# Kernel optimization log

Hardware: AMD Instinct MI355X
Metric: run time of the kernel (lower is better)

The kernel has to match this reference:

```python
import jax, jax.numpy as jnp
import numpy as np

T, B, C, U = 4000, 64, 64, 200
NEG_INF = jnp.float32(-1e30)


def setup_inputs() -> dict:
    key = jax.random.key(0)
    k1, k2 = jax.random.split(key)
    inputs = jax.random.normal(k1, (T, B, C), dtype=jnp.float32)  # time-major logits
    targets = jax.random.randint(k2, (B, U), 0, C, dtype=jnp.int32)
    return {"inputs": inputs, "targets": targets}


def reference(inputs, targets):
    # Transducer.forward: transitions is None -> log_softmax over classes.
    log_probs = jax.nn.log_softmax(inputs, axis=-1)  # [T, B, C]
    # emit[t, b, u] = log_probs[t, b, targets[b, u]]
    b_idx = jnp.arange(B)[:, None]  # [B, 1]
    emit = log_probs[:, b_idx, targets]  # [T, B, U]

    # ASG-style monotone alignment forward DP (no blank, repeats collapse):
    # alpha[t, u] = emit[t, u] + logsumexp(alpha[t-1, u], alpha[t-1, u-1])
    alpha0 = jnp.full((B, U), NEG_INF, dtype=inputs.dtype).at[:, 0].set(emit[0, :, 0])

    def step(alpha, emit_t):
        shifted = jnp.concatenate(
            [jnp.full((B, 1), NEG_INF, dtype=alpha.dtype), alpha[:, :-1]], axis=1
        )
        return emit_t + jnp.logaddexp(alpha, shifted), None

    alpha_T, _ = jax.lax.scan(step, alpha0, emit[1:])  # scan over T-1 frames
    losses = -alpha_T[:, U - 1]  # negated forward score per sample
    return jnp.mean(losses)  # TransducerLossFunction returns torch.mean(loss)
```

## Files before the change

### kernel.cpp

```cpp
#include <hip/hip_runtime.h>

#define T_DIM 4000
#define B_DIM 64
#define C_DIM 64
#define U_DIM 200
#define LOG2E 1.4426950408889634f
#define LN2 0.6931471805599453f

#define PAIRS 2000
#define PB_BYTES (PAIRS * 800)
#define NSLOT 20

__device__ __forceinline__ float hw_exp2(float x) { return __builtin_amdgcn_exp2f(x); }
__device__ __forceinline__ float hw_log2(float x) { return __builtin_amdgcn_logf(x); }

template <int CTRL>
__device__ __forceinline__ int dpp_i(int x) {
    return __builtin_amdgcn_update_dpp(0, x, CTRL, 0xF, 0xF, true);
}
template <int CTRL>
__device__ __forceinline__ float dpp_f(float x) {
    return __uint_as_float((unsigned)dpp_i<CTRL>((int)__float_as_uint(x)));
}

__device__ __forceinline__ unsigned rne_bf16(float v) {
    unsigned b = __float_as_uint(v);
    return b + 0x7FFFu + ((b >> 16) & 1u);
}

__global__ __launch_bounds__(256, 8) void prep_kernel(const float* __restrict__ in,
                                                      const int* __restrict__ tgt,
                                                      unsigned* __restrict__ eg,
                                                      float* __restrict__ out) {
    __shared__ unsigned short exh[16 * 8 * 68];
    __shared__ unsigned tgc[400];
    __shared__ float red[4];
    const int tid = threadIdx.x;
    const int bg = blockIdx.x & 7;
    const int tc = blockIdx.x >> 3;
    const int t0 = tc * 16, b0 = bg * 8;

    for (int o = tid; o < 400; o += 256) {
        int4 tv = ((const int4*)tgt)[bg * 400 + o];
        tgc[o] = (unsigned)(tv.x & 63) | ((unsigned)(tv.y & 63) << 8)
               | ((unsigned)(tv.z & 63) << 16) | ((unsigned)(tv.w & 63) << 24);
    }
    #pragma unroll
    for (int k = 0; k < 8; ++k) {
        int flat = k * 256 + tid;
        int t_l = flat >> 7, i = flat & 127, b_l = i >> 4, q = i & 15;
        float4 v = *(const float4*)(in + (size_t)(t0 + t_l) * 4096 + (b0 + b_l) * 64 + q * 4);
        unsigned ex0 = rne_bf16(hw_exp2(v.x * LOG2E));
        unsigned ex1 = rne_bf16(hw_exp2(v.y * LOG2E));
        unsigned ex2 = rne_bf16(hw_exp2(v.z * LOG2E));
        unsigned ex3 = rne_bf16(hw_exp2(v.w * LOG2E));
        uint2 pk;
        pk.x = (ex0 >> 16) | (ex1 & 0xFFFF0000u);
        pk.y = (ex2 >> 16) | (ex3 & 0xFFFF0000u);
        *(uint2*)&exh[(t_l * 8 + b_l) * 68 + q * 4] = pk;
    }
    __syncthreads();

    {
        float v = 0.0f;
        if (tid < 128) {
            const unsigned* p = (const unsigned*)&exh[tid * 68];
            float s = 0.0f;
            #pragma unroll
            for (int j = 0; j < 32; ++j) {
                unsigned u = p[j];
                s += __uint_as_float(u << 16) + __uint_as_float(u & 0xFFFF0000u);
            }
            v = hw_log2(s);
        }
        #pragma unroll
        for (int o = 32; o > 0; o >>= 1) v += __shfl_xor(v, o);
        if ((tid & 63) == 0) red[tid >> 6] = v;
    }

    {
        const int wv4 = tid >> 6;
        const int ln = tid & 63;
        for (int r = wv4; r < 64; r += 4) {
            int b_l = r & 7, tp_l = r >> 3;
            if (ln < 50) {
                unsigned tw = tgc[b_l * 50 + ln];
                int c0 = tw & 255, c1 = (tw >> 8) & 255, c2 = (tw >> 16) & 255, c3 = tw >> 24;
                const unsigned short* plo = &exh[(tp_l * 16 + b_l) * 68];
                const unsigned short* phi = plo + 8 * 68;
                uint4 w;
                w.x = (unsigned)plo[c0] | ((unsigned)plo[c1] << 16);
                w.y = (unsigned)plo[c2] | ((unsigned)plo[c3] << 16);
                w.z = (unsigned)phi[c0] | ((unsigned)phi[c1] << 16);
                w.w = (unsigned)phi[c2] | ((unsigned)phi[c3] << 16);
                *(uint4*)((char*)eg + (size_t)(b0 + b_l) * PB_BYTES
                          + (size_t)(tc * 8 + tp_l) * 800 + ln * 16) = w;
            }
        }
    }
    __syncthreads();
    if (tid == 0)
        atomicAdd(out, (red[0] + red[1] + red[2] + red[3]) * (LN2 / 64.0f));
}

struct ScanState { float A0, A1, A2, A3; int S, D; };

__device__ __forceinline__ void renorm(ScanState& st, int lane) {
    float m = fmaxf(fmaxf(st.A0, st.A1), fmaxf(st.A2, st.A3));
    int e = (int)((__float_as_uint(m) >> 23) & 0xFFu);
    int cand = st.S + e - 127;
    int snb = dpp_i<0x138>(st.S);
    if (lane == 0) snb = -(1 << 28);
    int snew = max(cand, snb);
    int k = st.S - snew;
    st.A0 = ldexpf(st.A0, k);
    st.A1 = ldexpf(st.A1, k);
    st.A2 = ldexpf(st.A2, k);
    st.A3 = ldexpf(st.A3, k);
    st.S = snew;
    st.D = min(dpp_i<0x138>(snew) - snew, 60);
}

__device__ __forceinline__ void step(ScanState& st, float e0, float e1, float e2, float e3) {
    float sh = ldexpf(dpp_f<0x138>(st.A3), st.D);
    sh = fminf(sh, 1.125899906842624e15f);
    float t0 = st.A0 + sh;
    float t1 = st.A1 + st.A0;
    float t2 = st.A2 + st.A1;
    float t3 = st.A3 + st.A2;
    st.A0 = e0 * t0; st.A1 = e1 * t1; st.A2 = e2 * t2; st.A3 = e3 * t3;
}

__device__ __forceinline__ void brenorm(ScanState& st) {
    float m = fmaxf(fmaxf(st.A0, st.A1), fmaxf(st.A2, st.A3));
    int e = (int)((__float_as_uint(m) >> 23) & 0xFFu);
    int cand = st.S + e - 127;
    int snb = dpp_i<0x130>(st.S);
    int snew = max(cand, snb);
    int k = st.S - snew;
    st.A0 = ldexpf(st.A0, k);
    st.A1 = ldexpf(st.A1, k);
    st.A2 = ldexpf(st.A2, k);
    st.A3 = ldexpf(st.A3, k);
    st.S = snew;
    st.D = min(dpp_i<0x130>(snew) - snew, 60);
}

__device__ __forceinline__ void bstep(ScanState& st, float e0, float e1, float e2, float e3) {
    float e4s = fminf(ldexpf(dpp_f<0x130>(e0), st.D), 1.125899906842624e15f);
    float b0n = dpp_f<0x130>(st.A0);
    float g0 = e0 * st.A0, g1 = e1 * st.A1, g2 = e2 * st.A2, g3 = e3 * st.A3;
    st.A0 = g0 + g1; st.A1 = g1 + g2; st.A2 = g2 + g3; st.A3 = g3 + e4s * b0n;
}

__device__ __forceinline__ ScanState scan_init(const float* in, const int* tgt, int lane, int b) {
    float v0 = in[b * 64 + (tgt[b * U_DIM] & 63)];
    ScanState st;
    st.A0 = (lane == 0) ? hw_exp2(v0 * LOG2E) : 0.0f;
    st.A1 = 0.0f; st.A2 = 0.0f; st.A3 = 0.0f;
    st.S = 0; st.D = 0;
    return st;
}

#define LO(x) __uint_as_float((x) << 16)
#define HI(x) __uint_as_float((x) & 0xFFFF0000u)

__global__ __launch_bounds__(128, 1) void scan2_kernel(const float* __restrict__ in,
                                                       const int* __restrict__ tgt,
                                                       const unsigned* __restrict__ eg,
                                                       float* __restrict__ out) {
    __shared__ float jb0[64], jb1[64], jb2[64], jb3[64];
    __shared__ int jsb[64];
    const int lane = threadIdx.x & 63;
    const int wv = threadIdx.x >> 6;
    const int b = blockIdx.x;
    const int lidx = (lane < 50) ? lane : 49;
    const char* egb = (const char*)eg + (size_t)b * PB_BYTES;

    ScanState st;
    if (wv == 1) {
        st.A0 = 0.0f; st.A1 = 0.0f; st.A2 = 0.0f;
        st.A3 = (lane == 49) ? 1.0f : 0.0f;
        st.S = 0; st.D = 0;
        int off = 1999 * 800 + lidx * 16;
        uint4 wb[NSLOT];
        #pragma unroll
        for (int j = 0; j < NSLOT; ++j) { wb[j] = *(const uint4*)(egb + off); off -= 800; }
        for (int k = 0; k < 49; ++k) {
            #pragma unroll
            for (int j = 0; j < NSLOT; ++j) {
                if ((j & 3) == 0) brenorm(st);
                uint4 w = wb[j];
                wb[j] = *(const uint4*)(egb + off); off -= 800;
                bstep(st, LO(w.z), HI(w.z), LO(w.w), HI(w.w));
                bstep(st, LO(w.x), HI(w.x), LO(w.y), HI(w.y));
            }
        }
        #pragma unroll
        for (int j = 0; j < NSLOT; ++j) {
            if ((j & 3) == 0) brenorm(st);
            uint4 w = wb[j];
            bstep(st, LO(w.z), HI(w.z), LO(w.w), HI(w.w));
            if (j < NSLOT - 1) bstep(st, LO(w.x), HI(w.x), LO(w.y), HI(w.y));
        }
        brenorm(st);
        jb0[lane] = st.A0; jb1[lane] = st.A1; jb2[lane] = st.A2; jb3[lane] = st.A3;
        jsb[lane] = st.S;
    } else {
        st = scan_init(in, tgt, lane, b);
        int off = 800 + lidx * 16;
        uint4 wb[NSLOT];
        #pragma unroll
        for (int j = 0; j < NSLOT; ++j) { wb[j] = *(const uint4*)(egb + off); off += 800; }
        uint2 h0 = *(const uint2*)(egb + lidx * 16 + 8);
        step(st, LO(h0.x), HI(h0.x), LO(h0.y), HI(h0.y));
        for (int k = 0; k < 49; ++k) {
            #pragma unroll
            for (int j = 0; j < NSLOT; ++j) {
                if ((j & 3) == 0) renorm(st, lane);
                uint4 w = wb[j];
                wb[j] = *(const uint4*)(egb + off); off += 800;
                step(st, LO(w.x), HI(w.x), LO(w.y), HI(w.y));
                step(st, LO(w.z), HI(w.z), LO(w.w), HI(w.w));
            }
        }
        #pragma unroll
        for (int j = 0; j < NSLOT; ++j) {
            if ((j & 3) == 0) renorm(st, lane);
            uint4 w = wb[j];
            step(st, LO(w.x), HI(w.x), LO(w.y), HI(w.y));
            if (j < NSLOT - 1) step(st, LO(w.z), HI(w.z), LO(w.w), HI(w.w));
        }
        renorm(st, lane);
    }
    __syncthreads();
    if (wv == 0) {
        float d = st.A0 * jb0[lane] + st.A1 * jb1[lane]
                + st.A2 * jb2[lane] + st.A3 * jb3[lane];
        float ll = (lane < 50) ? hw_log2(fmaxf(d, 1e-38f)) + (float)(st.S + jsb[lane])
                               : -1e30f;
        float mx = ll;
        #pragma unroll
        for (int o = 32; o > 0; o >>= 1) mx = fmaxf(mx, __shfl_xor(mx, o));
        float s = (lane < 50) ? hw_exp2(ll - mx) : 0.0f;
        #pragma unroll
        for (int o = 32; o > 0; o >>= 1) s += __shfl_xor(s, o);
        if (lane == 0) atomicAdd(out, -(mx + hw_log2(s)) * (LN2 / 64.0f));
    }
}

__global__ __launch_bounds__(256) void lse_sum_kernel(const float* __restrict__ in,
                                                      float* __restrict__ out) {
    const int lane = threadIdx.x & 63;
    const int w = threadIdx.x >> 6;
    const int wid = blockIdx.x * 4 + w;
    const int ROWS = (T_DIM * B_DIM) / 1024;
    const float* p = in + (size_t)wid * ROWS * 64 + lane;
    float acc = 0.0f;
    for (int i = 0; i < ROWS; i += 2) {
        float xa = p[(size_t)i * 64];
        float xb = p[(size_t)(i + 1) * 64];
        float ea = hw_exp2(xa * LOG2E);
        float eb = hw_exp2(xb * LOG2E);
        #pragma unroll
        for (int off = 32; off > 0; off >>= 1) {
            ea += __shfl_xor(ea, off);
            eb += __shfl_xor(eb, off);
        }
        acc += hw_log2(ea) + hw_log2(eb);
    }
    __shared__ float red[4];
    if (lane == 0) red[w] = acc;
    __syncthreads();
    if (threadIdx.x == 0)
        atomicAdd(out, (red[0] + red[1] + red[2] + red[3]) * (LN2 / 64.0f));
}

__global__ __launch_bounds__(64) void scan_fb(const float* __restrict__ in,
                                              const int* __restrict__ tgt,
                                              float* __restrict__ out) {
    const int lane = threadIdx.x;
    const int b = blockIdx.x;
    const int lidx = (lane < 50) ? lane : 49;
    int4 tg = ((const int4*)(tgt + b * U_DIM))[lidx];
    tg.x &= 63; tg.y &= 63; tg.z &= 63; tg.w &= 63;
    ScanState st = scan_init(in, tgt, lane, b);
    const char* inb = (const char*)in;
    int o0 = 16384 + b * 256 + tg.x * 4;
    int o1 = 16384 + b * 256 + tg.y * 4;
    int o2 = 16384 + b * 256 + tg.z * 4;
    int o3 = 16384 + b * 256 + tg.w * 4;
    const int m0 = 3999 * 16384 + b * 256 + tg.x * 4;
    const int m1 = m0 + (tg.y - tg.x) * 4;
    const int m2 = m0 + (tg.z - tg.x) * 4;
    const int m3 = m0 + (tg.w - tg.x) * 4;
    float f0[16], f1[16], f2[16], f3[16];
    #pragma unroll
    for (int j = 0; j < 16; ++j) {
        f0[j] = *(const float*)(inb + min(o0, m0)); o0 += 16384;
        f1[j] = *(const float*)(inb + min(o1, m1)); o1 += 16384;
        f2[j] = *(const float*)(inb + min(o2, m2)); o2 += 16384;
        f3[j] = *(const float*)(inb + min(o3, m3)); o3 += 16384;
    }
    for (int k = 0; k < 249; ++k) {
        #pragma unroll
        for (int j = 0; j < 16; ++j) {
            if (j == 0 || j == 8) renorm(st, lane);
            float e0 = hw_exp2(f0[j] * LOG2E);
            float e1 = hw_exp2(f1[j] * LOG2E);
            float e2 = hw_exp2(f2[j] * LOG2E);
            float e3 = hw_exp2(f3[j] * LOG2E);
            f0[j] = *(const float*)(inb + min(o0, m0)); o0 += 16384;
            f1[j] = *(const float*)(inb + min(o1, m1)); o1 += 16384;
            f2[j] = *(const float*)(inb + min(o2, m2)); o2 += 16384;
            f3[j] = *(const float*)(inb + min(o3, m3)); o3 += 16384;
            step(st, e0, e1, e2, e3);
        }
    }
    #pragma unroll
    for (int j = 0; j < 15; ++j) {
        if (j == 0 || j == 8) renorm(st, lane);
        float e0 = hw_exp2(f0[j] * LOG2E);
        float e1 = hw_exp2(f1[j] * LOG2E);
        float e2 = hw_exp2(f2[j] * LOG2E);
        float e3 = hw_exp2(f3[j] * LOG2E);
        step(st, e0, e1, e2, e3);
    }
    if (lane == 49) {
        float a2 = hw_log2(fmaxf(st.A3, 1e-38f)) + (float)st.S;
        atomicAdd(out, -a2 * (LN2 / 64.0f));
    }
}

extern "C" void kernel_launch(void* const* d_in, const int* in_sizes, int n_in,
                              void* d_out, int out_size, void* d_ws, size_t ws_size,
                              hipStream_t stream) {
    const float* inputs = (const float*)d_in[0];
    const int* targets = (const int*)d_in[1];
    float* out = (float*)d_out;

    (void)hipMemsetAsync(out, 0, sizeof(float), stream);

    const size_t eg_bytes = (size_t)B_DIM * PB_BYTES;
    if (ws_size >= eg_bytes) {
        unsigned* eg = (unsigned*)d_ws;
        prep_kernel<<<2000, 256, 0, stream>>>(inputs, targets, eg, out);
        scan2_kernel<<<B_DIM, 128, 0, stream>>>(inputs, targets, eg, out);
    } else {
        scan_fb<<<B_DIM, 64, 0, stream>>>(inputs, targets, out);
        lse_sum_kernel<<<256, 256, 0, stream>>>(inputs, out);
    }
}
```

Baseline: 189.8 us.

## Interleave forward and backward scans in a single wave per batch

The forward and backward DP scans used to run in two separate waves of a 128-thread block, joined through shared memory and a barrier. Now one 64-lane wave runs both chains, interleaving forward and backward steps so each dependent chain hides the other's latency (ILP instead of wave-level parallelism). This drops the LDS exchange and the __syncthreads, but doubles the per-wave register footprint (two 20-slot prefetch buffers) and halves the waves per CU, so total latency now depends on how well the interleaving fills the issue slots.

Result: slower. 253.6 us (+33.6%).

```diff
diff --git a/kernel.cpp b/kernel.cpp
--- a/kernel.cpp
+++ b/kernel.cpp
@@ -165,88 +165,71 @@
 #define LO(x) __uint_as_float((x) << 16)
 #define HI(x) __uint_as_float((x) & 0xFFFF0000u)
 
-__global__ __launch_bounds__(128, 1) void scan2_kernel(const float* __restrict__ in,
-                                                       const int* __restrict__ tgt,
-                                                       const unsigned* __restrict__ eg,
-                                                       float* __restrict__ out) {
-    __shared__ float jb0[64], jb1[64], jb2[64], jb3[64];
-    __shared__ int jsb[64];
-    const int lane = threadIdx.x & 63;
-    const int wv = threadIdx.x >> 6;
+__global__ __launch_bounds__(64, 1) void scan2_kernel(const float* __restrict__ in,
+                                                      const int* __restrict__ tgt,
+                                                      const unsigned* __restrict__ eg,
+                                                      float* __restrict__ out) {
+    const int lane = threadIdx.x;
     const int b = blockIdx.x;
     const int lidx = (lane < 50) ? lane : 49;
     const char* egb = (const char*)eg + (size_t)b * PB_BYTES;
 
-    ScanState st;
-    if (wv == 1) {
-        st.A0 = 0.0f; st.A1 = 0.0f; st.A2 = 0.0f;
-        st.A3 = (lane == 49) ? 1.0f : 0.0f;
-        st.S = 0; st.D = 0;
-        int off = 1999 * 800 + lidx * 16;
-        uint4 wb[NSLOT];
-        #pragma unroll
-        for (int j = 0; j < NSLOT; ++j) { wb[j] = *(const uint4*)(egb + off); off -= 800; }
-        for (int k = 0; k < 49; ++k) {
-            #pragma unroll
-            for (int j = 0; j < NSLOT; ++j) {
-                if ((j & 3) == 0) brenorm(st);
-                uint4 w = wb[j];
-                wb[j] = *(const uint4*)(egb + off); off -= 800;
-                bstep(st, LO(w.z), HI(w.z), LO(w.w), HI(w.w));
-                bstep(st, LO(w.x), HI(w.x), LO(w.y), HI(w.y));
-            }
-        }
+    ScanState sb;
+    sb.A0 = 0.0f; sb.A1 = 0.0f; sb.A2 = 0.0f;
+    sb.A3 = (lane == 49) ? 1.0f : 0.0f;
+    sb.S = 0; sb.D = 0;
+    ScanState sf = scan_init(in, tgt, lane, b);
+
+    int offF = 800 + lidx * 16;
+    int offB = 1999 * 800 + lidx * 16;
+    uint4 wf[NSLOT], wk[NSLOT];
+    #pragma unroll
+    for (int j = 0; j < NSLOT; ++j) {
+        wf[j] = *(const uint4*)(egb + offF); offF += 800;
+        wk[j] = *(const uint4*)(egb + offB); offB -= 800;
+    }
+    uint2 h0 = *(const uint2*)(egb + lidx * 16 + 8);
+    step(sf, LO(h0.x), HI(h0.x), LO(h0.y), HI(h0.y));
+
+    for (int k = 0; k < 49; ++k) {
         #pragma unroll
         for (int j = 0; j < NSLOT; ++j) {
-            if ((j & 3) == 0) brenorm(st);
-            uint4 w = wb[j];
-            bstep(st, LO(w.z), HI(w.z), LO(w.w), HI(w.w));
-            if (j < NSLOT - 1) bstep(st, LO(w.x), HI(w.x), LO(w.y), HI(w.y));
-        }
-        brenorm(st);
-        jb0[lane] = st.A0; jb1[lane] = st.A1; jb2[lane] = st.A2; jb3[lane] = st.A3;
-        jsb[lane] = st.S;
-    } else {
-        st = scan_init(in, tgt, lane, b);
-        int off = 800 + lidx * 16;
-        uint4 wb[NSLOT];
-        #pragma unroll
-        for (int j = 0; j < NSLOT; ++j) { wb[j] = *(const uint4*)(egb + off); off += 800; }
-        uint2 h0 = *(const uint2*)(egb + lidx * 16 + 8);
-        step(st, LO(h0.x), HI(h0.x), LO(h0.y), HI(h0.y));
-        for (int k = 0; k < 49; ++k) {
-            #pragma unroll
-            for (int j = 0; j < NSLOT; ++j) {
-                if ((j & 3) == 0) renorm(st, lane);
-                uint4 w = wb[j];
-                wb[j] = *(const uint4*)(egb + off); off += 800;
-                step(st, LO(w.x), HI(w.x), LO(w.y), HI(w.y));
-                step(st, LO(w.z), HI(w.z), LO(w.w), HI(w.w));
-            }
-        }
-        #pragma unroll
-        for (int j = 0; j < NSLOT; ++j) {
-            if ((j & 3) == 0) renorm(st, lane);
-            uint4 w = wb[j];
-            step(st, LO(w.x), HI(w.x), LO(w.y), HI(w.y));
-            if (j < NSLOT - 1) step(st, LO(w.z), HI(w.z), LO(w.w), HI(w.w));
-        }
-        renorm(st, lane);
-    }
-    __syncthreads();
-    if (wv == 0) {
-        float d = st.A0 * jb0[lane] + st.A1 * jb1[lane]
-                + st.A2 * jb2[lane] + st.A3 * jb3[lane];
-        float ll = (lane < 50) ? hw_log2(fmaxf(d, 1e-38f)) + (float)(st.S + jsb[lane])
-                               : -1e30f;
-        float mx = ll;
-        #pragma unroll
-        for (int o = 32; o > 0; o >>= 1) mx = fmaxf(mx, __shfl_xor(mx, o));
-        float s = (lane < 50) ? hw_exp2(ll - mx) : 0.0f;
-        #pragma unroll
-        for (int o = 32; o > 0; o >>= 1) s += __shfl_xor(s, o);
-        if (lane == 0) atomicAdd(out, -(mx + hw_log2(s)) * (LN2 / 64.0f));
-    }
+            if ((j & 3) == 0) { renorm(sf, lane); brenorm(sb); }
+            uint4 a = wf[j];
+            wf[j] = *(const uint4*)(egb + offF); offF += 800;
+            uint4 c = wk[j];
+            wk[j] = *(const uint4*)(egb + offB); offB -= 800;
+            step(sf, LO(a.x), HI(a.x), LO(a.y), HI(a.y));
+            bstep(sb, LO(c.z), HI(c.z), LO(c.w), HI(c.w));
+            step(sf, LO(a.z), HI(a.z), LO(a.w), HI(a.w));
+            bstep(sb, LO(c.x), HI(c.x), LO(c.y), HI(c.y));
+        }
+    }
+    #pragma unroll
+    for (int j = 0; j < NSLOT; ++j) {
+        if ((j & 3) == 0) { renorm(sf, lane); brenorm(sb); }
+        uint4 a = wf[j];
+        uint4 c = wk[j];
+        step(sf, LO(a.x), HI(a.x), LO(a.y), HI(a.y));
+        bstep(sb, LO(c.z), HI(c.z), LO(c.w), HI(c.w));
+        if (j < NSLOT - 1) {
+            step(sf, LO(a.z), HI(a.z), LO(a.w), HI(a.w));
+            bstep(sb, LO(c.x), HI(c.x), LO(c.y), HI(c.y));
+        }
+    }
+    renorm(sf, lane);
+    brenorm(sb);
+
+    float d = sf.A0 * sb.A0 + sf.A1 * sb.A1 + sf.A2 * sb.A2 + sf.A3 * sb.A3;
+    float ll = (lane < 50) ? hw_log2(fmaxf(d, 1e-38f)) + (float)(sf.S + sb.S)
+                           : -1e30f;
+    float mx = ll;
+    #pragma unroll
+    for (int o = 32; o > 0; o >>= 1) mx = fmaxf(mx, __shfl_xor(mx, o));
+    float s = (lane < 50) ? hw_exp2(ll - mx) : 0.0f;
+    #pragma unroll
+    for (int o = 32; o > 0; o >>= 1) s += __shfl_xor(s, o);
+    if (lane == 0) atomicAdd(out, -(mx + hw_log2(s)) * (LN2 / 64.0f));
 }
 
 __global__ __launch_bounds__(256) void lse_sum_kernel(const float* __restrict__ in,
@@ -345,7 +328,7 @@
     if (ws_size >= eg_bytes) {
         unsigned* eg = (unsigned*)d_ws;
         prep_kernel<<<2000, 256, 0, stream>>>(inputs, targets, eg, out);
-        scan2_kernel<<<B_DIM, 128, 0, stream>>>(inputs, targets, eg, out);
+        scan2_kernel<<<B_DIM, 64, 0, stream>>>(inputs, targets, eg, out);
     } else {
         scan_fb<<<B_DIM, 64, 0, stream>>>(inputs, targets, out);
         lse_sum_kernel<<<256, 256, 0, stream>>>(inputs, out);
```
